# Kernel tuning notes

Hardware: AMD Instinct MI355X
Metric: run time of the kernel (lower is better)

The kernel has to match this reference:

```python
import jax, jax.numpy as jnp
import numpy as np

N = 65536      # number of points
D = 3          # spatial dimension (init arg 'dimension')
C = 64         # feature channels
K = 16         # neighbors returned by faiss knn search
BLOCK = 512    # query block size for chunked brute-force distances
GRID = 128     # spatial_size


def setup_inputs() -> dict:
    key = jax.random.key(0)
    k1, k2 = jax.random.split(key)
    coords = jax.random.randint(k1, (N, D), 0, GRID, dtype=jnp.int32)
    features = jax.random.normal(k2, (N, C), dtype=jnp.float32)
    return {"coords": coords, "features": features}


def reference(coords, features):
    """Brute-force KNN over integer point coords (faiss-equivalent exact L2
    search), then sparse input-layer construction: for each point, gather the
    features of its K nearest neighbors and sum them (SCN InputLayer mode=3)."""
    cf = coords.astype(jnp.float32)                 # [N, D]
    db_sq = jnp.sum(cf * cf, axis=1)                # [N]

    n_blocks = N // BLOCK
    queries = cf.reshape(n_blocks, BLOCK, D)

    def step(_, q):                                 # q: [BLOCK, D]
        q_sq = jnp.sum(q * q, axis=1)               # [BLOCK]
        # squared L2 distances to all database points: [BLOCK, N]
        dist = q_sq[:, None] - 2.0 * (q @ cf.T) + db_sq[None, :]
        _, idx = jax.lax.top_k(-dist, K)            # [BLOCK, K] nearest indices
        nb = features[idx]                          # irregular gather [BLOCK, K, C]
        return None, jnp.sum(nb, axis=1)            # mode=3: sum duplicates/neighbors

    _, out = jax.lax.scan(step, None, queries)      # [n_blocks, BLOCK, C]
    return out.reshape(N, C)
```

## Files before the change

kernel.cpp:

```cpp
#include <hip/hip_runtime.h>


typedef unsigned int uint;
typedef unsigned short ushort;
typedef short short2v __attribute__((ext_vector_type(2)));

#define NPTS   65536
#define NCELL  32768

static __device__ inline short2v u2s(uint v) { union { uint u; short2v s; } c; c.u = v; return c.s; }
static __device__ inline uint s2u(short2v v) { union { uint u; short2v s; } c; c.s = v; return c.u; }

static __device__ inline int dot2acc(short2v a, short2v b, int c) {
#if __has_builtin(__builtin_amdgcn_sdot2)
    return __builtin_amdgcn_sdot2(a, b, c, false);
#else
    return (int)a.x * (int)b.x + (int)a.y * (int)b.y + c;
#endif
}

__global__ __launch_bounds__(256) void cell_count(const int* __restrict__ coords,
                                                  uint* __restrict__ counts) {
    int i = blockIdx.x * 256 + threadIdx.x;
    int x = coords[3 * i + 0], y = coords[3 * i + 1], z = coords[3 * i + 2];
    int cell = (x >> 2) | ((y >> 2) << 5) | ((z >> 2) << 10);
    atomicAdd(&counts[cell], 1u);
}

__global__ __launch_bounds__(1024) void cell_scan(const uint* __restrict__ counts,
                                                  uint* __restrict__ starts,
                                                  uint* __restrict__ cursors) {
    __shared__ uint wsum[16];
    int t = threadIdx.x;
    int lane = t & 63, wv = t >> 6;
    uint4 c[8];
    uint s = 0;
#pragma unroll
    for (int j = 0; j < 8; ++j) {
        c[j] = reinterpret_cast<const uint4*>(counts)[t * 8 + j];
        s += c[j].x + c[j].y + c[j].z + c[j].w;
    }
    uint v = s;
#pragma unroll
    for (int off = 1; off < 64; off <<= 1) {
        uint u = __shfl_up(v, off, 64);
        if (lane >= off) v += u;
    }
    if (lane == 63) wsum[wv] = v;
    __syncthreads();
    if (wv == 0 && lane < 16) {
        uint w = wsum[lane];
#pragma unroll
        for (int off = 1; off < 16; off <<= 1) {
            uint u = __shfl_up(w, off, 64);
            if (lane >= off) w += u;
        }
        wsum[lane] = w;
    }
    __syncthreads();
    uint base = v - s + (wv > 0 ? wsum[wv - 1] : 0u);
#pragma unroll
    for (int j = 0; j < 8; ++j) {
        uint4 st;
        st.x = base;
        st.y = st.x + c[j].x;
        st.z = st.y + c[j].y;
        st.w = st.z + c[j].z;
        base = st.w + c[j].w;
        reinterpret_cast<uint4*>(starts)[t * 8 + j]  = st;
        reinterpret_cast<uint4*>(cursors)[t * 8 + j] = st;
    }
    if (t == 1023) starts[NCELL] = wsum[15];
}

__global__ __launch_bounds__(256) void cell_scatter(const int* __restrict__ coords,
                                                    uint* __restrict__ cursors,
                                                    uint2* __restrict__ sorted) {
    int i = blockIdx.x * 256 + threadIdx.x;
    int x = coords[3 * i + 0], y = coords[3 * i + 1], z = coords[3 * i + 2];
    int cell = (x >> 2) | ((y >> 2) << 5) | ((z >> 2) << 10);
    uint pos = atomicAdd(&cursors[cell], 1u);
    sorted[pos] = make_uint2((uint)(x | (y << 16)), (uint)(i | (z << 16)));
}

__global__ __launch_bounds__(128, 8) void knn_search(const uint* __restrict__ starts,
                                                     const uint2* __restrict__ sorted,
                                                     const float* __restrict__ feat,
                                                     float* __restrict__ out) {
    int blk  = (blockIdx.x & 7) * 512 + (blockIdx.x >> 3);
    int wave = threadIdx.x >> 6;
    int lane = threadIdx.x & 63;
    int qslot = lane & 7;
    int slice = lane >> 3;
    int qpos = blk * 16 + wave * 8 + qslot;

    uint2 me = sorted[qpos];
    uint qxy = me.x;
    uint qzp = me.y & 0xFFFF0000u;
    uint qidx = me.y & 0xFFFFu;
    int qx = (int)(me.x & 0xFFFFu);
    int qy = (int)(me.x >> 16);
    int qz = (int)(me.y >> 16);
    int cx = qx >> 2, cy = qy >> 2, cz = qz >> 2;

    uint k[16];
#pragma unroll
    for (int j = 0; j < 16; ++j) k[j] = 0xFFFFFFFFu;

    auto insert1 = [&](uint2 pt) {
        short2v A = u2s(pt.x) - u2s(qxy);
        short2v B = u2s(pt.y) - u2s(qzp);
        uint Bu = s2u(B);
        short2v Bm = u2s(Bu & 0xFFFF0000u);
        int d2 = dot2acc(A, A, dot2acc(Bm, Bm, 0));
        uint key = ((uint)d2 << 16) + (Bu & 0xFFFFu);
#pragma unroll
        for (int j = 15; j >= 1; --j)
            asm("v_med3_u32 %0, %1, %2, %3"
                : "=v"(k[j]) : "v"(k[j - 1]), "v"(k[j]), "v"(key));
        k[0] = min(k[0], key);
    };

    auto scan8 = [&](uint p0, uint p1) {
        for (uint p = p0 + (uint)slice; p < p1; p += 8u) insert1(sorted[p]);
    };

    auto merge = [&](int mask) {
        uint b[16], c[16];
#pragma unroll
        for (int j = 0; j < 16; ++j) b[j] = __shfl_xor(k[j], mask, 64);
#pragma unroll
        for (int j = 0; j < 16; ++j) c[j] = min(k[j], b[15 - j]);
#pragma unroll
        for (int d = 8; d >= 1; d >>= 1) {
#pragma unroll
            for (int i = 0; i < 16; ++i) {
                if ((i & d) == 0) {
                    uint lo = min(c[i], c[i + d]);
                    uint hi = max(c[i], c[i + d]);
                    c[i] = lo;
                    c[i + d] = hi;
                }
            }
        }
#pragma unroll
        for (int j = 0; j < 16; ++j) k[j] = c[j];
    };
    auto merge_all = [&]() { merge(8); merge(16); merge(32); };

    int xa = min(max(cx - ((qx & 3) < 2 ? 2 : 1), 0), 28);
    int ya = min(max(cy - ((qy & 3) < 2 ? 2 : 1), 0), 28);
    int za = min(max(cz - ((qz & 3) < 2 ? 2 : 1), 0), 28);

    {
        int rbA = ((ya + (slice & 3)) << 5) | ((za + (slice >> 2)) << 10);
        int rbB = ((ya + (slice & 3)) << 5) | ((za + 2 + (slice >> 2)) << 10);
        uint pA = starts[rbA + xa], eA = starts[rbA + xa + 4];
        uint pB = starts[rbB + xa], eB = starts[rbB + xa + 4];
        while (__any((pA < eA) || (pB < eB))) {
            bool a = pA < eA, b = pB < eB;
            uint2 ptA, ptB;
            if (a) ptA = sorted[pA];
            if (b) ptB = sorted[pB];
            pA += a ? 1u : 0u;
            pB += b ? 1u : 0u;
            if (a) insert1(ptA);
            if (b) insert1(ptB);
        }
    }
    merge_all();

    bool redo = (k[15] >> 16) >= 49u;
    if (__any(redo)) {
        if (redo || slice != 0) {
#pragma unroll
            for (int j = 0; j < 16; ++j) k[j] = 0xFFFFFFFFu;
        }
        if (redo) {
            int xl = max(cx - 2, 0), xh = min(cx + 2, 31);
            int yl = max(cy - 2, 0), yh = min(cy + 2, 31);
            int zl = max(cz - 2, 0), zh = min(cz + 2, 31);
            for (int z = zl; z <= zh; ++z)
                for (int y = yl; y <= yh; ++y) {
                    int rb = (y << 5) | (z << 10);
                    scan8(starts[rb + xl], starts[rb + xh + 1]);
                }
        }
        merge_all();
        for (int r = 3; r < 32; ++r) {
            uint b = (uint)(4 * r - 3);
            bool active = (k[15] >> 16) >= b * b;
            if (!__any(active)) break;
            if (slice != 0) {
#pragma unroll
                for (int j = 0; j < 16; ++j) k[j] = 0xFFFFFFFFu;
            }
            if (active) {
                int z0 = cz - r < 0 ? 0 : cz - r;
                int z1 = cz + r > 31 ? 31 : cz + r;
                for (int z = z0; z <= z1; ++z) {
                    bool zface = (z == cz - r) || (z == cz + r);
                    int y0 = cy - r < 0 ? 0 : cy - r;
                    int y1 = cy + r > 31 ? 31 : cy + r;
                    for (int y = y0; y <= y1; ++y) {
                        bool face = zface || (y == cy - r) || (y == cy + r);
                        int rb = (y << 5) | (z << 10);
                        if (face) {
                            int x0 = cx - r < 0 ? 0 : cx - r;
                            int x1 = cx + r > 31 ? 31 : cx + r;
                            scan8(starts[rb + x0], starts[rb + x1 + 1]);
                        } else {
                            int xL = cx - r;
                            if (xL >= 0) scan8(starts[rb + xL], starts[rb + xL + 1]);
                            int xR = cx + r;
                            if (xR <= 31) scan8(starts[rb + xR], starts[rb + xR + 1]);
                        }
                    }
                }
            }
            merge_all();
        }
    }

    uint ki[16];
#pragma unroll
    for (int j = 0; j < 16; ++j) ki[j] = k[j] & 0xFFFFu;

    int ch = lane & 15;
    int qg = lane >> 4;
#pragma unroll
    for (int p = 0; p < 2; ++p) {
        int qs = p * 4 + qg;
        uint qorig = __shfl(qidx, qs, 64);
        float4 acc = make_float4(0.f, 0.f, 0.f, 0.f);
#pragma unroll
        for (int j = 0; j < 16; ++j) {
            uint nj = __shfl(ki[j], qs, 64);
            float4 v = reinterpret_cast<const float4*>(feat)[nj * 16u + (uint)ch];
            acc.x += v.x; acc.y += v.y; acc.z += v.z; acc.w += v.w;
        }
        reinterpret_cast<float4*>(out)[qorig * 16u + (uint)ch] = acc;
    }
}

extern "C" void kernel_launch(void* const* d_in, const int* in_sizes, int n_in,
                              void* d_out, int out_size, void* d_ws, size_t ws_size,
                              hipStream_t stream) {
    const int*   coords = (const int*)d_in[0];
    const float* feat   = (const float*)d_in[1];
    float*       out    = (float*)d_out;

    uint* W = (uint*)d_ws;
    uint*   counts  = W;
    uint*   starts  = W + 32768;
    uint*   cursors = W + 65540;
    uint2*  sorted  = (uint2*)(W + 98308);

    hipMemsetAsync(counts, 0, NCELL * sizeof(uint), stream);
    cell_count<<<NPTS / 256, 256, 0, stream>>>(coords, counts);
    cell_scan<<<1, 1024, 0, stream>>>(counts, starts, cursors);
    cell_scatter<<<NPTS / 256, 256, 0, stream>>>(coords, cursors, sorted);
    knn_search<<<4096, 128, 0, stream>>>(starts, sorted, feat, out);
}
```

Before: 70.36 us.

## Fuse grid build kernels into one persistent kernel with software grid barriers

```diff
diff --git a/kernel.cpp b/kernel.cpp
--- a/kernel.cpp
+++ b/kernel.cpp
@@ -7,6 +7,8 @@
 
 #define NPTS   65536
 #define NCELL  32768
+#define BBLK   256
+#define BTPB   256
 
 static __device__ inline short2v u2s(uint v) { union { uint u; short2v s; } c; c.u = v; return c.s; }
 static __device__ inline uint s2u(short2v v) { union { uint u; short2v s; } c; c.s = v; return c.u; }
@@ -19,66 +21,76 @@
 #endif
 }
 
-__global__ __launch_bounds__(256) void cell_count(const int* __restrict__ coords,
-                                                  uint* __restrict__ counts) {
-    int i = blockIdx.x * 256 + threadIdx.x;
+static __device__ __forceinline__ void gridbar(uint* bar, uint target) {
+    __syncthreads();
+    if (threadIdx.x == 0) {
+        __hip_atomic_fetch_add(bar, 1u, __ATOMIC_ACQ_REL, __HIP_MEMORY_SCOPE_AGENT);
+        while (__hip_atomic_load(bar, __ATOMIC_ACQUIRE, __HIP_MEMORY_SCOPE_AGENT) < target)
+            __builtin_amdgcn_s_sleep(1);
+    }
+    __syncthreads();
+}
+
+__global__ __launch_bounds__(BTPB) void build(const int* __restrict__ coords,
+                                              uint* __restrict__ bar,
+                                              uint* __restrict__ counts,
+                                              uint* __restrict__ starts,
+                                              uint* __restrict__ cursors,
+                                              uint2* __restrict__ sorted) {
+    __shared__ uint wsum[4];
+    __shared__ uint rsum[4];
+    int b = blockIdx.x, tid = threadIdx.x;
+    int i = b * BTPB + tid;
+    int lane = tid & 63, wv = tid >> 6;
+
     int x = coords[3 * i + 0], y = coords[3 * i + 1], z = coords[3 * i + 2];
     int cell = (x >> 2) | ((y >> 2) << 5) | ((z >> 2) << 10);
     atomicAdd(&counts[cell], 1u);
-}
-
-__global__ __launch_bounds__(1024) void cell_scan(const uint* __restrict__ counts,
-                                                  uint* __restrict__ starts,
-                                                  uint* __restrict__ cursors) {
-    __shared__ uint wsum[16];
-    int t = threadIdx.x;
-    int lane = t & 63, wv = t >> 6;
-    uint4 c[8];
-    uint s = 0;
-#pragma unroll
-    for (int j = 0; j < 8; ++j) {
-        c[j] = reinterpret_cast<const uint4*>(counts)[t * 8 + j];
-        s += c[j].x + c[j].y + c[j].z + c[j].w;
-    }
-    uint v = s;
-#pragma unroll
-    for (int off = 1; off < 64; off <<= 1) {
-        uint u = __shfl_up(v, off, 64);
-        if (lane >= off) v += u;
-    }
-    if (lane == 63) wsum[wv] = v;
-    __syncthreads();
-    if (wv == 0 && lane < 16) {
-        uint w = wsum[lane];
-#pragma unroll
-        for (int off = 1; off < 16; off <<= 1) {
-            uint u = __shfl_up(w, off, 64);
-            if (lane >= off) w += u;
-        }
-        wsum[lane] = w;
-    }
-    __syncthreads();
-    uint base = v - s + (wv > 0 ? wsum[wv - 1] : 0u);
-#pragma unroll
-    for (int j = 0; j < 8; ++j) {
-        uint4 st;
-        st.x = base;
-        st.y = st.x + c[j].x;
-        st.z = st.y + c[j].y;
-        st.w = st.z + c[j].z;
-        base = st.w + c[j].w;
-        reinterpret_cast<uint4*>(starts)[t * 8 + j]  = st;
-        reinterpret_cast<uint4*>(cursors)[t * 8 + j] = st;
-    }
-    if (t == 1023) starts[NCELL] = wsum[15];
-}
-
-__global__ __launch_bounds__(256) void cell_scatter(const int* __restrict__ coords,
-                                                    uint* __restrict__ cursors,
-                                                    uint2* __restrict__ sorted) {
-    int i = blockIdx.x * 256 + threadIdx.x;
-    int x = coords[3 * i + 0], y = coords[3 * i + 1], z = coords[3 * i + 2];
-    int cell = (x >> 2) | ((y >> 2) << 5) | ((z >> 2) << 10);
+    gridbar(bar, BBLK);
+
+    uint* bsums = (uint*)sorted;
+    uint c = 0, excl = 0;
+    if (b < 128) {
+        int t2 = b * 256 + tid;
+        c = __hip_atomic_load(&counts[t2], __ATOMIC_RELAXED, __HIP_MEMORY_SCOPE_AGENT);
+        uint v = c;
+#pragma unroll
+        for (int off = 1; off < 64; off <<= 1) {
+            uint u = __shfl_up(v, off, 64);
+            if (lane >= off) v += u;
+        }
+        if (lane == 63) wsum[wv] = v;
+        __syncthreads();
+        uint woff = 0, btot = 0;
+#pragma unroll
+        for (int j = 0; j < 4; ++j) {
+            uint w = wsum[j];
+            woff += (j < wv) ? w : 0u;
+            btot += w;
+        }
+        excl = woff + v - c;
+        if (tid == 0)
+            __hip_atomic_store(&bsums[b], btot, __ATOMIC_RELAXED, __HIP_MEMORY_SCOPE_AGENT);
+    }
+    gridbar(bar, 2 * BBLK);
+
+    if (b < 128) {
+        uint s = 0;
+        if (tid < 128 && tid < b)
+            s = __hip_atomic_load(&bsums[tid], __ATOMIC_RELAXED, __HIP_MEMORY_SCOPE_AGENT);
+#pragma unroll
+        for (int off = 32; off; off >>= 1) s += __shfl_xor(s, off, 64);
+        if (lane == 0) rsum[wv] = s;
+        __syncthreads();
+        uint blockoff = rsum[0] + rsum[1] + rsum[2] + rsum[3];
+        int t2 = b * 256 + tid;
+        uint st = blockoff + excl;
+        starts[t2] = st;
+        __hip_atomic_store(&cursors[t2], st, __ATOMIC_RELAXED, __HIP_MEMORY_SCOPE_AGENT);
+        if (t2 == NCELL - 1) starts[NCELL] = st + c;
+    }
+    gridbar(bar, 3 * BBLK);
+
     uint pos = atomicAdd(&cursors[cell], 1u);
     sorted[pos] = make_uint2((uint)(x | (y << 16)), (uint)(i | (z << 16)));
 }
@@ -125,27 +137,28 @@
         for (uint p = p0 + (uint)slice; p < p1; p += 8u) insert1(sorted[p]);
     };
 
-    auto merge = [&](int mask) {
-        uint b[16], c[16];
+    auto merge_min = [&](int mask) {
+        uint b[16];
 #pragma unroll
         for (int j = 0; j < 16; ++j) b[j] = __shfl_xor(k[j], mask, 64);
 #pragma unroll
-        for (int j = 0; j < 16; ++j) c[j] = min(k[j], b[15 - j]);
+        for (int j = 0; j < 16; ++j) k[j] = min(k[j], b[15 - j]);
+    };
+    auto clean = [&]() {
 #pragma unroll
         for (int d = 8; d >= 1; d >>= 1) {
 #pragma unroll
             for (int i = 0; i < 16; ++i) {
                 if ((i & d) == 0) {
-                    uint lo = min(c[i], c[i + d]);
-                    uint hi = max(c[i], c[i + d]);
-                    c[i] = lo;
-                    c[i + d] = hi;
+                    uint lo = min(k[i], k[i + d]);
+                    uint hi = max(k[i], k[i + d]);
+                    k[i] = lo;
+                    k[i + d] = hi;
                 }
             }
         }
-#pragma unroll
-        for (int j = 0; j < 16; ++j) k[j] = c[j];
-    };
+    };
+    auto merge = [&](int mask) { merge_min(mask); clean(); };
     auto merge_all = [&]() { merge(8); merge(16); merge(32); };
 
     int xa = min(max(cx - ((qx & 3) < 2 ? 2 : 1), 0), 28);
@@ -168,10 +181,14 @@
             if (b) insert1(ptB);
         }
     }
-    merge_all();
-
-    bool redo = (k[15] >> 16) >= 49u;
+    merge(8); merge(16); merge_min(32);
+    uint mx = k[0];
+#pragma unroll
+    for (int j = 1; j < 16; ++j) mx = max(mx, k[j]);
+
+    bool redo = (mx >> 16) >= 49u;
     if (__any(redo)) {
+        clean();
         if (redo || slice != 0) {
 #pragma unroll
             for (int j = 0; j < 16; ++j) k[j] = 0xFFFFFFFFu;
@@ -251,14 +268,13 @@
     float*       out    = (float*)d_out;
 
     uint* W = (uint*)d_ws;
-    uint*   counts  = W;
-    uint*   starts  = W + 32768;
-    uint*   cursors = W + 65540;
-    uint2*  sorted  = (uint2*)(W + 98308);
-
-    hipMemsetAsync(counts, 0, NCELL * sizeof(uint), stream);
-    cell_count<<<NPTS / 256, 256, 0, stream>>>(coords, counts);
-    cell_scan<<<1, 1024, 0, stream>>>(counts, starts, cursors);
-    cell_scatter<<<NPTS / 256, 256, 0, stream>>>(coords, cursors, sorted);
+    uint*  bar     = W;
+    uint*  counts  = W + 8;
+    uint*  starts  = W + 32776;
+    uint*  cursors = W + 65548;
+    uint2* sorted  = (uint2*)(W + 98316);
+
+    hipMemsetAsync(W, 0, (8 + NCELL) * sizeof(uint), stream);
+    build<<<BBLK, BTPB, 0, stream>>>(coords, bar, counts, starts, cursors, sorted);
     knn_search<<<4096, 128, 0, stream>>>(starts, sorted, feat, out);
 }
```

Measured after the change: 87.32 us. 24.1% more time.
